# Performance work log

Measured on AMD Instinct MI355X. Metric: run time of the kernel, lower is better.

Reference implementation:

```python
import jax, jax.numpy as jnp
import numpy as np
from jax import lax

N_TAPS = 27  # 3x3x3 kernel

def _gather_one(xb, ti, hi, wi):
    # xb: (C,T,H,W); ti/hi/wi: (T,H,W) int32. Zero-fill outside bounds.
    C, T, H, W = xb.shape
    valid = (ti >= 0) & (ti < T) & (hi >= 0) & (hi < H) & (wi >= 0) & (wi < W)
    lin = (jnp.clip(ti, 0, T - 1) * H + jnp.clip(hi, 0, H - 1)) * W + jnp.clip(wi, 0, W - 1)
    v = jnp.take(xb.reshape(C, -1), lin.reshape(-1), axis=1).reshape(C, T, H, W)
    return v * valid.astype(xb.dtype)

_gather = jax.vmap(_gather_one)  # over batch

def _trilinear(x, t, h, w):
    # x: (B,C,T,H,W); t/h/w: (B,T,H,W) float sample coordinates.
    t0, h0, w0 = jnp.floor(t), jnp.floor(h), jnp.floor(w)
    lt, lh, lw = t - t0, h - h0, w - w0
    t0i, h0i, w0i = t0.astype(jnp.int32), h0.astype(jnp.int32), w0.astype(jnp.int32)
    acc = 0.0
    for ti, wt in ((t0i, 1.0 - lt), (t0i + 1, lt)):
        for hi, wh in ((h0i, 1.0 - lh), (h0i + 1, lh)):
            for wi, ww in ((w0i, 1.0 - lw), (w0i + 1, lw)):
                acc = acc + _gather(x, ti, hi, wi) * (wt * wh * ww)[:, None]
    return acc  # (B,C,T,H,W)

def _deform_conv3d(x, offset_w, offset_b, weight):
    # x: (B,Cin,T,H,W). Offset layout: (B, 3, 27, T, H, W), axis1=(dt,dh,dw),
    # tap index k = kt*9 + kh*3 + kw. stride=1, padding=1, dilation=1, no bias.
    off = lax.conv_general_dilated(
        x, offset_w, (1, 1, 1), [(1, 1)] * 3,
        dimension_numbers=("NCDHW", "OIDHW", "NCDHW"))
    off = off + offset_b[None, :, None, None, None]
    B, _, T, H, W = off.shape
    off = off.reshape(B, 3, N_TAPS, T, H, W)
    tg = jnp.arange(T, dtype=x.dtype)[:, None, None]
    hg = jnp.arange(H, dtype=x.dtype)[None, :, None]
    wg = jnp.arange(W, dtype=x.dtype)[None, None, :]
    out = jnp.zeros((B, weight.shape[0], T, H, W), x.dtype)
    for k in range(N_TAPS):
        kt, kh, kw = k // 9, (k // 3) % 3, k % 3
        t = tg + (kt - 1) + off[:, 0, k]
        h = hg + (kh - 1) + off[:, 1, k]
        w = wg + (kw - 1) + off[:, 2, k]
        s = _trilinear(x, t, h, w)  # (B,Cin,T,H,W)
        out = out + jnp.einsum('bcthw,oc->bothw', s, weight[:, :, kt, kh, kw])
    return out

def setup_inputs() -> dict:
    key = jax.random.key(0)
    ks = jax.random.split(key, 4)
    B, T, C, H, W = 1, 4, 64, 128, 128
    x = jax.random.normal(ks[0], (B, T, C, H, W), jnp.float32)
    # small init scale keeps predicted offsets in a realistic +-2px range
    offset_w = jax.random.normal(ks[1], (3 * N_TAPS, C, 3, 3, 3), jnp.float32) * 0.02
    offset_b = jnp.zeros((3 * N_TAPS,), jnp.float32)
    weight = jax.random.normal(ks[2], (C, C, 3, 3, 3), jnp.float32) * 0.02
    gamma = jax.random.normal(ks[3], (1,), jnp.float32) * 0.1
    return {"x": x, "offset_w": offset_w, "offset_b": offset_b,
            "weight": weight, "gamma": gamma}

def reference(x, offset_w, offset_b, weight, gamma):
    xp = jnp.transpose(x, (0, 2, 1, 3, 4))  # (B,C,T,H,W)
    xc = _deform_conv3d(xp, offset_w, offset_b, weight)
    return gamma[0] * jnp.transpose(xc, (0, 2, 1, 3, 4)) + x
```

## Files before the change

kernel.cpp:

```cpp
#include <hip/hip_runtime.h>
#include <cmath>

#define Cc 64
#define Hh 128
#define Ww 128
#define HW_ 16384
#define THW_ 65536
#define CHW_ 1048576
#define NT 27

typedef unsigned short ushort_t;
typedef _Float16 f16x2 __attribute__((ext_vector_type(2)));
typedef _Float16 f16x8 __attribute__((ext_vector_type(8)));
typedef __fp16 fp16x2_alt __attribute__((ext_vector_type(2)));
typedef float floatx4 __attribute__((ext_vector_type(4)));
typedef unsigned uint4v __attribute__((ext_vector_type(4)));

union U32H2 { unsigned u; f16x2 h; };

static __device__ inline ushort_t f2h(float f) {
  union { _Float16 h; ushort_t u; } v;
  v.h = (_Float16)f;
  return v.u;
}

static __device__ inline unsigned pk2(float a) {
  union { fp16x2_alt h; unsigned u; } v;
  v.h = __builtin_amdgcn_cvt_pkrtz(a, a);
  return v.u;
}

#if defined(__has_builtin)
#if __has_builtin(__builtin_amdgcn_make_buffer_rsrc) && __has_builtin(__builtin_amdgcn_raw_buffer_load_b32) && __has_builtin(__builtin_amdgcn_raw_buffer_load_b128)
#define USE_BUF 1
#endif
#endif
#ifndef USE_BUF
#define USE_BUF 0
#endif

struct XtBuf {
#if USE_BUF
  __amdgpu_buffer_rsrc_t r;
#else
  const char* p;
#endif
};

static __device__ inline XtBuf mkbuf(const ushort_t* xt) {
  XtBuf b;
#if USE_BUF
  b.r = __builtin_amdgcn_make_buffer_rsrc((void*)xt, (short)0, 8388608, 0x00020000);
#else
  b.p = (const char*)xt;
#endif
  return b;
}

static __device__ inline uint4v xload4(const XtBuf& b, unsigned voff) {
#if USE_BUF
  return __builtin_amdgcn_raw_buffer_load_b128(b.r, (int)voff, 0, 0);
#else
  return *(const uint4v*)(b.p + voff);
#endif
}


__global__ __launch_bounds__(256) void prep(
    const float* __restrict__ offset_w,
    const float* __restrict__ weight,
    ushort_t* __restrict__ w2frag,
    ushort_t* __restrict__ wfrag)
{
  int e = blockIdx.x * 256 + threadIdx.x;
  if (e < 165888) {
    int j = e & 7, ln = (e >> 3) & 63, kh2 = (e >> 9) & 1, r = e >> 10;
    int ot = r % 6, k = r / 6;
    int oc = ot * 16 + (ln & 15);
    int c  = kh2 * 32 + (ln >> 4) * 8 + j;
    float v = (oc < 81) ? offset_w[(oc * 64 + c) * 27 + k] : 0.f;
    w2frag[e] = f2h(v);
  }
  if (e < 110592) {
    int j = e & 7, ln = (e >> 3) & 63, kh2 = (e >> 9) & 1, r = e >> 10;
    int ot = r & 3, k = r >> 2;
    int o = ot * 16 + (ln & 15);
    int c = kh2 * 32 + (ln >> 4) * 8 + j;
    wfrag[e] = f2h(weight[(o * 64 + c) * 27 + k]);
  }
}

__global__ __launch_bounds__(256) void transpose_x(
    const float* __restrict__ x, ushort_t* __restrict__ xt)
{
  __shared__ float tile[64][65];
  int b = blockIdx.x;
  int wblk = b & 1;
  int th = b >> 1;
  int h = th & 127;
  int t = th >> 7;
  int w0 = wblk * 64;
  int lane = threadIdx.x & 63;
  int quad = threadIdx.x >> 6;
  #pragma unroll
  for (int cc = 0; cc < 16; ++cc) {
    int c = cc * 4 + quad;
    tile[c][lane] = x[t * CHW_ + c * HW_ + h * Ww + w0 + lane];
  }
  __syncthreads();
  #pragma unroll
  for (int ww = 0; ww < 16; ++ww) {
    int w = ww * 4 + quad;
    xt[(size_t)(t * HW_ + h * Ww + w0 + w) * 64 + lane] = f2h(tile[lane][w]);
  }
}

__global__ __launch_bounds__(256, 4) void offconv(
    const ushort_t* __restrict__ xt,
    const ushort_t* __restrict__ w2frag,
    const float* __restrict__ ob,
    float* __restrict__ off)
{
  __shared__ __align__(16) char lds[24960];
  ushort_t* S = (ushort_t*)lds;
  float* Dbuf = (float*)lds;
  int lane = threadIdx.x & 63;
  int wavei = __builtin_amdgcn_readfirstlane(threadIdx.x >> 6);
  int quad = lane >> 4;
  int m16 = lane & 15;
  int g8 = lane >> 3;
  unsigned coff = (unsigned)((lane & 7) * 16);
  int bid0 = blockIdx.x;
  int p0 = ((bid0 & 7) * 128 + (bid0 >> 3)) * 64;
  int t = p0 >> 14;
  int h = (p0 >> 7) & 127;
  int w0 = p0 & 127;
  XtBuf xb = mkbuf(xt);

  floatx4 acc[6];
  #pragma unroll
  for (int i = 0; i < 6; ++i) acc[i] = (floatx4){0.f, 0.f, 0.f, 0.f};

  uint4v pd[2];

  auto issue = [&](int k) {
    int kt = k / 9, kh = (k / 3) % 3, kw = k % 3;
    int ts = t + kt - 1, hs = h + kh - 1;
    int tsc = min(max(ts, 0), 3);
    int hsc = min(max(hs, 0), 127);
    int sbase = tsc * HW_ + hsc * Ww;
    #pragma unroll
    for (int b = 0; b < 2; ++b) {
      int prow = wavei * 16 + b * 8 + g8;
      int wc = w0 + prow + kw - 1;
      int wcc = min(max(wc, 0), 127);
      pd[b] = xload4(xb, ((unsigned)(sbase + wcc) << 7) + coff);
    }
  };

  issue(0);
  #pragma unroll 1
  for (int k = 0; k < NT; ++k) {
    int kt = k / 9, kh = (k / 3) % 3, kw = k % 3;
    int ts = t + kt - 1, hs = h + kh - 1;
    bool rowok = ((unsigned)ts < 4u) && ((unsigned)hs < 128u);
    #pragma unroll
    for (int b = 0; b < 2; ++b) {
      int prow = wavei * 16 + b * 8 + g8;
      int wc = w0 + prow + kw - 1;
      bool ok = rowok && ((unsigned)wc < 128u);
      uint4v v = pd[b];
      if (!ok) v = (uint4v){0u, 0u, 0u, 0u};
      *(uint4v*)((char*)S + prow * 144 + coff) = v;
    }
    issue(k + 1 < NT ? k + 1 : NT - 1);
    const ushort_t* srow = S + (wavei * 16 + m16) * 72 + quad * 8;
    f16x8 af0 = *(const f16x8*)srow;
    f16x8 af1 = *(const f16x8*)(srow + 32);
    #pragma unroll
    for (int ot = 0; ot < 6; ++ot) {
      const ushort_t* wb = w2frag + (size_t)((k * 6 + ot) * 2) * 512 + lane * 8;
      f16x8 b0 = *(const f16x8*)(wb);
      f16x8 b1 = *(const f16x8*)(wb + 512);
      acc[ot] = __builtin_amdgcn_mfma_f32_16x16x32_f16(af0, b0, acc[ot], 0, 0, 0);
      acc[ot] = __builtin_amdgcn_mfma_f32_16x16x32_f16(af1, b1, acc[ot], 0, 0, 0);
    }
  }
  __syncthreads();
  #pragma unroll
  for (int ot = 0; ot < 6; ++ot)
    #pragma unroll
    for (int r = 0; r < 4; ++r)
      Dbuf[(ot * 16 + m16) * 65 + wavei * 16 + quad * 4 + r] = acc[ot][r];
  __syncthreads();
  for (int i = threadIdx.x; i < 81 * 64; i += 256) {
    int oc = i >> 6, p = i & 63;
    off[(size_t)oc * THW_ + p0 + p] = Dbuf[oc * 65 + p] + ob[oc];
  }
}

#define SITE(W, D, A0, A1, A2, A3) \
  { U32H2 wu; wu.u = (W); U32H2 q0, q1, q2, q3; \
    q0.u = (D)[0]; q1.u = (D)[1]; q2.u = (D)[2]; q3.u = (D)[3]; \
    A0 += wu.h * q0.h; A1 += wu.h * q1.h; A2 += wu.h * q2.h; A3 += wu.h * q3.h; }

__global__ __launch_bounds__(256, 4) void deform(
    const float* __restrict__ x,
    const ushort_t* __restrict__ xt,
    const float* __restrict__ off,
    const ushort_t* __restrict__ wfrag,
    const float* __restrict__ gamma,
    float* __restrict__ out)
{
  __shared__ __align__(16) char lds[17408];
  ushort_t* S = (ushort_t*)lds;
  unsigned* msite0 = (unsigned*)(lds + 9216);
  unsigned* msite1 = (unsigned*)(lds + 11264);
  unsigned* mwt0   = (unsigned*)(lds + 13312);
  unsigned* mwt1   = (unsigned*)(lds + 15360);
  float* Dbuf = (float*)lds;
  int lane = threadIdx.x & 63;
  int wavei = __builtin_amdgcn_readfirstlane(threadIdx.x >> 6);
  int quad = lane >> 4;
  int m16 = lane & 15;
  int g8 = lane >> 3;
  unsigned coff = (unsigned)((lane & 7) * 16);
  int bid0 = blockIdx.x;
  int p0 = ((bid0 & 7) * 128 + (bid0 >> 3)) * 64;
  int t = p0 >> 14;
  int h = (p0 >> 7) & 127;
  int w0 = p0 & 127;
  XtBuf xb = mkbuf(xt);

  floatx4 acc[4];
  #pragma unroll
  for (int i = 0; i < 4; ++i) acc[i] = (floatx4){0.f, 0.f, 0.f, 0.f};

  int pl = wavei * 16 + m16;
  int pm = p0 + pl;
  int aq = quad >> 1, bq = quad & 1;
  int rowA = wavei * 16 + g8;
  int rowB = rowA + 8;
  const float* offT = off + pm;

  uint4v stA[8], stB[8];

  auto meta = [&](int kk, float dtv, float dhv, float dwv) {
    unsigned* ms = (kk & 1) ? msite1 : msite0;
    unsigned* mw = (kk & 1) ? mwt1 : mwt0;
    int kt = kk / 9, kh = (kk / 3) % 3, kw = kk % 3;
    float tf = (float)(t + kt - 1) + dtv;
    float hf = (float)(h + kh - 1) + dhv;
    float wf = (float)(w0 + pl + kw - 1) + dwv;
    float tF = floorf(tf), hF = floorf(hf), wF = floorf(wf);
    float lt = tf - tF, lh_ = hf - hF, lw_ = wf - wF;
    int t0 = (int)tF, h0 = (int)hF, wq_ = (int)wF;
    int ti = t0 + aq;
    float wt_ = (aq ? lt : 1.f - lt) * (((unsigned)ti < 4u) ? 1.f : 0.f);
    int tic = min(max(ti, 0), 3);
    int hi = h0 + bq;
    float wh_ = (bq ? lh_ : 1.f - lh_) * (((unsigned)hi < 128u) ? 1.f : 0.f);
    int hic = min(max(hi, 0), 127);
    int base2 = tic * HW_ + hic * Ww;
    float bw = wt_ * wh_;
    int wi0 = wq_;
    float ww0 = (1.f - lw_) * (((unsigned)wi0 < 128u) ? 1.f : 0.f);
    int wi0c = min(max(wi0, 0), 127);
    int wi1 = wq_ + 1;
    float ww1 = lw_ * (((unsigned)wi1 < 128u) ? 1.f : 0.f);
    int wi1c = min(max(wi1, 0), 127);
    uint2 sp_;
    sp_.x = (unsigned)(base2 + wi0c) << 7;
    sp_.y = (unsigned)(base2 + wi1c) << 7;
    *(uint2*)&ms[pl * 8 + quad * 2] = sp_;
    uint2 wp_;
    wp_.x = pk2(bw * ww0);
    wp_.y = pk2(bw * ww1);
    *(uint2*)&mw[pl * 8 + quad * 2] = wp_;
  };

  auto issueA = [&](int kk) {
    const unsigned* ms = (kk & 1) ? msite1 : msite0;
    const uint4* sp = (const uint4*)&ms[rowA * 8];
    uint4 s0 = sp[0], s1 = sp[1];
    stA[0] = xload4(xb, s0.x + coff);
    stA[1] = xload4(xb, s0.y + coff);
    stA[2] = xload4(xb, s0.z + coff);
    stA[3] = xload4(xb, s0.w + coff);
    stA[4] = xload4(xb, s1.x + coff);
    stA[5] = xload4(xb, s1.y + coff);
    stA[6] = xload4(xb, s1.z + coff);
    stA[7] = xload4(xb, s1.w + coff);
  };
  auto issueB = [&](int kk) {
    const unsigned* ms = (kk & 1) ? msite1 : msite0;
    const uint4* sp = (const uint4*)&ms[rowB * 8];
    uint4 s0 = sp[0], s1 = sp[1];
    stB[0] = xload4(xb, s0.x + coff);
    stB[1] = xload4(xb, s0.y + coff);
    stB[2] = xload4(xb, s0.z + coff);
    stB[3] = xload4(xb, s0.w + coff);
    stB[4] = xload4(xb, s1.x + coff);
    stB[5] = xload4(xb, s1.y + coff);
    stB[6] = xload4(xb, s1.z + coff);
    stB[7] = xload4(xb, s1.w + coff);
  };

  auto consumeA = [&](int kk) {
    const unsigned* mw = (kk & 1) ? mwt1 : mwt0;
    const uint4* wp = (const uint4*)&mw[rowA * 8];
    uint4 w03 = wp[0], w47 = wp[1];
    U32H2 z; z.u = 0;
    f16x2 e0 = z.h, e1 = z.h, e2 = z.h, e3 = z.h;
    f16x2 o0 = z.h, o1 = z.h, o2 = z.h, o3 = z.h;
    SITE(w03.x, stA[0], e0, e1, e2, e3)
    SITE(w03.y, stA[1], o0, o1, o2, o3)
    SITE(w03.z, stA[2], e0, e1, e2, e3)
    SITE(w03.w, stA[3], o0, o1, o2, o3)
    SITE(w47.x, stA[4], e0, e1, e2, e3)
    SITE(w47.y, stA[5], o0, o1, o2, o3)
    SITE(w47.z, stA[6], e0, e1, e2, e3)
    SITE(w47.w, stA[7], o0, o1, o2, o3)
    U32H2 r0, r1, r2, r3;
    r0.h = e0 + o0; r1.h = e1 + o1; r2.h = e2 + o2; r3.h = e3 + o3;
    uint4v res = {r0.u, r1.u, r2.u, r3.u};
    *(uint4v*)((char*)S + rowA * 144 + coff) = res;
  };
  auto consumeB = [&](int kk) {
    const unsigned* mw = (kk & 1) ? mwt1 : mwt0;
    const uint4* wp = (const uint4*)&mw[rowB * 8];
    uint4 w03 = wp[0], w47 = wp[1];
    U32H2 z; z.u = 0;
    f16x2 e0 = z.h, e1 = z.h, e2 = z.h, e3 = z.h;
    f16x2 o0 = z.h, o1 = z.h, o2 = z.h, o3 = z.h;
    SITE(w03.x, stB[0], e0, e1, e2, e3)
    SITE(w03.y, stB[1], o0, o1, o2, o3)
    SITE(w03.z, stB[2], e0, e1, e2, e3)
    SITE(w03.w, stB[3], o0, o1, o2, o3)
    SITE(w47.x, stB[4], e0, e1, e2, e3)
    SITE(w47.y, stB[5], o0, o1, o2, o3)
    SITE(w47.z, stB[6], e0, e1, e2, e3)
    SITE(w47.w, stB[7], o0, o1, o2, o3)
    U32H2 r0, r1, r2, r3;
    r0.h = e0 + o0; r1.h = e1 + o1; r2.h = e2 + o2; r3.h = e3 + o3;
    uint4v res = {r0.u, r1.u, r2.u, r3.u};
    *(uint4v*)((char*)S + rowB * 144 + coff) = res;
  };

  float dt0 = offT[(size_t)(0 * NT + 0) * THW_];
  float dh0 = offT[(size_t)(1 * NT + 0) * THW_];
  float dw0 = offT[(size_t)(2 * NT + 0) * THW_];
  meta(0, dt0, dh0, dw0);
  issueA(0);

  #pragma unroll 1
  for (int k = 0; k < NT; ++k) {
    int kn = (k + 1 < NT) ? k + 1 : NT - 1;
    float dt_n = offT[(size_t)(0 * NT + kn) * THW_];
    float dh_n = offT[(size_t)(1 * NT + kn) * THW_];
    float dw_n = offT[(size_t)(2 * NT + kn) * THW_];

    issueB(k);
    __builtin_amdgcn_sched_barrier(0);
    consumeA(k);
    meta(kn, dt_n, dh_n, dw_n);
    consumeB(k);
    issueA(kn);
    __builtin_amdgcn_sched_barrier(0);

    const ushort_t* srow = S + (wavei * 16 + m16) * 72 + quad * 8;
    f16x8 af0 = *(const f16x8*)srow;
    f16x8 af1 = *(const f16x8*)(srow + 32);
    #pragma unroll
    for (int ot = 0; ot < 4; ++ot) {
      const ushort_t* wb = wfrag + (size_t)((k * 4 + ot) * 2) * 512 + lane * 8;
      f16x8 b0 = *(const f16x8*)(wb);
      f16x8 b1 = *(const f16x8*)(wb + 512);
      acc[ot] = __builtin_amdgcn_mfma_f32_16x16x32_f16(af0, b0, acc[ot], 0, 0, 0);
      acc[ot] = __builtin_amdgcn_mfma_f32_16x16x32_f16(af1, b1, acc[ot], 0, 0, 0);
    }
  }
  __syncthreads();
  #pragma unroll
  for (int ot = 0; ot < 4; ++ot)
    #pragma unroll
    for (int r = 0; r < 4; ++r)
      Dbuf[(ot * 16 + m16) * 65 + wavei * 16 + quad * 4 + r] = acc[ot][r];
  __syncthreads();
  float g = gamma[0];
  for (int i = threadIdx.x; i < 64 * 64; i += 256) {
    int oc = i >> 6, p = i & 63;
    size_t oi = (size_t)t * CHW_ + (size_t)oc * HW_ + (size_t)h * Ww + w0 + p;
    out[oi] = fmaf(g, Dbuf[oc * 65 + p], x[oi]);
  }
}

extern "C" void kernel_launch(void* const* d_in, const int* in_sizes, int n_in,
                              void* d_out, int out_size, void* d_ws, size_t ws_size,
                              hipStream_t stream) {
  (void)in_sizes; (void)n_in; (void)out_size; (void)ws_size;
  const float* x        = (const float*)d_in[0];
  const float* offset_w = (const float*)d_in[1];
  const float* offset_b = (const float*)d_in[2];
  const float* weight   = (const float*)d_in[3];
  const float* gamma    = (const float*)d_in[4];
  float* out = (float*)d_out;
  float* wsf = (float*)d_ws;
  float*    off    = wsf;
  ushort_t* xt     = (ushort_t*)(wsf + 5308416);
  ushort_t* wfrag  = (ushort_t*)(wsf + 7405568);
  ushort_t* w2frag = (ushort_t*)(wsf + 7460864);

  hipLaunchKernelGGL(prep, dim3(648), dim3(256), 0, stream,
                     offset_w, weight, w2frag, wfrag);
  hipLaunchKernelGGL(transpose_x, dim3(1024), dim3(256), 0, stream, x, xt);
  hipLaunchKernelGGL(offconv, dim3(1024), dim3(256), 0, stream,
                     xt, w2frag, offset_b, off);
  hipLaunchKernelGGL(deform, dim3(1024), dim3(256), 0, stream,
                     x, xt, off, wfrag, gamma, out);
}
```

Before: 224.6 us.

## Fuse offset convolution into deformable conv kernel, keeping offsets in LDS

Merges the offset-prediction conv kernel and the deformable sampling kernel into one launch. Each block computes its 81 offset channels for its 64 pixels with MFMA, adds the bias, and keeps them in shared memory instead of writing them to and reading them back from a global workspace. This removes a global round trip of about 21 MB and one kernel launch. In exchange LDS per block grows to about 38 KB, which may lower occupancy, and register pressure rises because both phases live in one kernel.

```diff
diff --git a/kernel.cpp b/kernel.cpp
--- a/kernel.cpp
+++ b/kernel.cpp
@@ -115,14 +115,27 @@
   }
 }
 
-__global__ __launch_bounds__(256, 4) void offconv(
+#define SITE(W, D, A0, A1, A2, A3) \
+  { U32H2 wu; wu.u = (W); U32H2 q0, q1, q2, q3; \
+    q0.u = (D)[0]; q1.u = (D)[1]; q2.u = (D)[2]; q3.u = (D)[3]; \
+    A0 += wu.h * q0.h; A1 += wu.h * q1.h; A2 += wu.h * q2.h; A3 += wu.h * q3.h; }
+
+__global__ __launch_bounds__(256, 4) void fused(
+    const float* __restrict__ x,
     const ushort_t* __restrict__ xt,
     const ushort_t* __restrict__ w2frag,
     const float* __restrict__ ob,
-    float* __restrict__ off)
+    const ushort_t* __restrict__ wfrag,
+    const float* __restrict__ gamma,
+    float* __restrict__ out)
 {
-  __shared__ __align__(16) char lds[24960];
+  __shared__ __align__(16) char lds[38480];
   ushort_t* S = (ushort_t*)lds;
+  unsigned* msite0 = (unsigned*)(lds + 9216);
+  unsigned* msite1 = (unsigned*)(lds + 11264);
+  unsigned* mwt0   = (unsigned*)(lds + 13312);
+  unsigned* mwt1   = (unsigned*)(lds + 15360);
+  float* Obuf = (float*)(lds + 17408);
   float* Dbuf = (float*)lds;
   int lane = threadIdx.x & 63;
   int wavei = __builtin_amdgcn_readfirstlane(threadIdx.x >> 6);
@@ -137,111 +150,76 @@
   int w0 = p0 & 127;
   XtBuf xb = mkbuf(xt);
 
-  floatx4 acc[6];
-  #pragma unroll
-  for (int i = 0; i < 6; ++i) acc[i] = (floatx4){0.f, 0.f, 0.f, 0.f};
-
-  uint4v pd[2];
-
-  auto issue = [&](int k) {
-    int kt = k / 9, kh = (k / 3) % 3, kw = k % 3;
-    int ts = t + kt - 1, hs = h + kh - 1;
-    int tsc = min(max(ts, 0), 3);
-    int hsc = min(max(hs, 0), 127);
-    int sbase = tsc * HW_ + hsc * Ww;
+  {
+    floatx4 acc[6];
     #pragma unroll
-    for (int b = 0; b < 2; ++b) {
-      int prow = wavei * 16 + b * 8 + g8;
-      int wc = w0 + prow + kw - 1;
-      int wcc = min(max(wc, 0), 127);
-      pd[b] = xload4(xb, ((unsigned)(sbase + wcc) << 7) + coff);
+    for (int i = 0; i < 6; ++i) acc[i] = (floatx4){0.f, 0.f, 0.f, 0.f};
+
+    uint4v pd[2];
+
+    auto issue = [&](int k) {
+      int kt = k / 9, kh = (k / 3) % 3, kw = k % 3;
+      int ts = t + kt - 1, hs = h + kh - 1;
+      int tsc = min(max(ts, 0), 3);
+      int hsc = min(max(hs, 0), 127);
+      int sbase = tsc * HW_ + hsc * Ww;
+      #pragma unroll
+      for (int b = 0; b < 2; ++b) {
+        int prow = wavei * 16 + b * 8 + g8;
+        int wc = w0 + prow + kw - 1;
+        int wcc = min(max(wc, 0), 127);
+        pd[b] = xload4(xb, ((unsigned)(sbase + wcc) << 7) + coff);
+      }
+    };
+
+    issue(0);
+    #pragma unroll 1
+    for (int k = 0; k < NT; ++k) {
+      int kt = k / 9, kh = (k / 3) % 3, kw = k % 3;
+      int ts = t + kt - 1, hs = h + kh - 1;
+      bool rowok = ((unsigned)ts < 4u) && ((unsigned)hs < 128u);
+      #pragma unroll
+      for (int b = 0; b < 2; ++b) {
+        int prow = wavei * 16 + b * 8 + g8;
+        int wc = w0 + prow + kw - 1;
+        bool ok = rowok && ((unsigned)wc < 128u);
+        uint4v v = pd[b];
+        if (!ok) v = (uint4v){0u, 0u, 0u, 0u};
+        *(uint4v*)((char*)S + prow * 144 + coff) = v;
+      }
+      if (k + 1 < NT) issue(k + 1);
+      const ushort_t* srow = S + (wavei * 16 + m16) * 72 + quad * 8;
+      f16x8 af0 = *(const f16x8*)srow;
+      f16x8 af1 = *(const f16x8*)(srow + 32);
+      #pragma unroll
+      for (int ot = 0; ot < 6; ++ot) {
+        const ushort_t* wb = w2frag + (size_t)((k * 6 + ot) * 2) * 512 + lane * 8;
+        f16x8 b0 = *(const f16x8*)(wb);
+        f16x8 b1 = *(const f16x8*)(wb + 512);
+        acc[ot] = __builtin_amdgcn_mfma_f32_16x16x32_f16(af0, b0, acc[ot], 0, 0, 0);
+        acc[ot] = __builtin_amdgcn_mfma_f32_16x16x32_f16(af1, b1, acc[ot], 0, 0, 0);
+      }
     }
-  };
-
-  issue(0);
-  #pragma unroll 1
-  for (int k = 0; k < NT; ++k) {
-    int kt = k / 9, kh = (k / 3) % 3, kw = k % 3;
-    int ts = t + kt - 1, hs = h + kh - 1;
-    bool rowok = ((unsigned)ts < 4u) && ((unsigned)hs < 128u);
-    #pragma unroll
-    for (int b = 0; b < 2; ++b) {
-      int prow = wavei * 16 + b * 8 + g8;
-      int wc = w0 + prow + kw - 1;
-      bool ok = rowok && ((unsigned)wc < 128u);
-      uint4v v = pd[b];
-      if (!ok) v = (uint4v){0u, 0u, 0u, 0u};
-      *(uint4v*)((char*)S + prow * 144 + coff) = v;
-    }
-    issue(k + 1 < NT ? k + 1 : NT - 1);
-    const ushort_t* srow = S + (wavei * 16 + m16) * 72 + quad * 8;
-    f16x8 af0 = *(const f16x8*)srow;
-    f16x8 af1 = *(const f16x8*)(srow + 32);
     #pragma unroll
     for (int ot = 0; ot < 6; ++ot) {
-      const ushort_t* wb = w2frag + (size_t)((k * 6 + ot) * 2) * 512 + lane * 8;
-      f16x8 b0 = *(const f16x8*)(wb);
-      f16x8 b1 = *(const f16x8*)(wb + 512);
-      acc[ot] = __builtin_amdgcn_mfma_f32_16x16x32_f16(af0, b0, acc[ot], 0, 0, 0);
-      acc[ot] = __builtin_amdgcn_mfma_f32_16x16x32_f16(af1, b1, acc[ot], 0, 0, 0);
+      int oc = ot * 16 + m16;
+      if (oc < 81) {
+        float bv = ob[oc];
+        #pragma unroll
+        for (int r = 0; r < 4; ++r)
+          Obuf[oc * 65 + wavei * 16 + quad * 4 + r] = acc[ot][r] + bv;
+      }
     }
   }
-  __syncthreads();
-  #pragma unroll
-  for (int ot = 0; ot < 6; ++ot)
-    #pragma unroll
-    for (int r = 0; r < 4; ++r)
-      Dbuf[(ot * 16 + m16) * 65 + wavei * 16 + quad * 4 + r] = acc[ot][r];
-  __syncthreads();
-  for (int i = threadIdx.x; i < 81 * 64; i += 256) {
-    int oc = i >> 6, p = i & 63;
-    off[(size_t)oc * THW_ + p0 + p] = Dbuf[oc * 65 + p] + ob[oc];
-  }
-}
-
-#define SITE(W, D, A0, A1, A2, A3) \
-  { U32H2 wu; wu.u = (W); U32H2 q0, q1, q2, q3; \
-    q0.u = (D)[0]; q1.u = (D)[1]; q2.u = (D)[2]; q3.u = (D)[3]; \
-    A0 += wu.h * q0.h; A1 += wu.h * q1.h; A2 += wu.h * q2.h; A3 += wu.h * q3.h; }
-
-__global__ __launch_bounds__(256, 4) void deform(
-    const float* __restrict__ x,
-    const ushort_t* __restrict__ xt,
-    const float* __restrict__ off,
-    const ushort_t* __restrict__ wfrag,
-    const float* __restrict__ gamma,
-    float* __restrict__ out)
-{
-  __shared__ __align__(16) char lds[17408];
-  ushort_t* S = (ushort_t*)lds;
-  unsigned* msite0 = (unsigned*)(lds + 9216);
-  unsigned* msite1 = (unsigned*)(lds + 11264);
-  unsigned* mwt0   = (unsigned*)(lds + 13312);
-  unsigned* mwt1   = (unsigned*)(lds + 15360);
-  float* Dbuf = (float*)lds;
-  int lane = threadIdx.x & 63;
-  int wavei = __builtin_amdgcn_readfirstlane(threadIdx.x >> 6);
-  int quad = lane >> 4;
-  int m16 = lane & 15;
-  int g8 = lane >> 3;
-  unsigned coff = (unsigned)((lane & 7) * 16);
-  int bid0 = blockIdx.x;
-  int p0 = ((bid0 & 7) * 128 + (bid0 >> 3)) * 64;
-  int t = p0 >> 14;
-  int h = (p0 >> 7) & 127;
-  int w0 = p0 & 127;
-  XtBuf xb = mkbuf(xt);
 
   floatx4 acc[4];
   #pragma unroll
   for (int i = 0; i < 4; ++i) acc[i] = (floatx4){0.f, 0.f, 0.f, 0.f};
 
   int pl = wavei * 16 + m16;
-  int pm = p0 + pl;
   int aq = quad >> 1, bq = quad & 1;
   int rowA = wavei * 16 + g8;
   int rowB = rowA + 8;
-  const float* offT = off + pm;
 
   uint4v stA[8], stB[8];
 
@@ -347,25 +325,27 @@
     *(uint4v*)((char*)S + rowB * 144 + coff) = res;
   };
 
-  float dt0 = offT[(size_t)(0 * NT + 0) * THW_];
-  float dh0 = offT[(size_t)(1 * NT + 0) * THW_];
-  float dw0 = offT[(size_t)(2 * NT + 0) * THW_];
-  meta(0, dt0, dh0, dw0);
+  {
+    float dt0 = Obuf[(0 * NT + 0) * 65 + pl];
+    float dh0 = Obuf[(1 * NT + 0) * 65 + pl];
+    float dw0 = Obuf[(2 * NT + 0) * 65 + pl];
+    meta(0, dt0, dh0, dw0);
+  }
   issueA(0);
 
   #pragma unroll 1
   for (int k = 0; k < NT; ++k) {
     int kn = (k + 1 < NT) ? k + 1 : NT - 1;
-    float dt_n = offT[(size_t)(0 * NT + kn) * THW_];
-    float dh_n = offT[(size_t)(1 * NT + kn) * THW_];
-    float dw_n = offT[(size_t)(2 * NT + kn) * THW_];
+    float dt_n = Obuf[(0 * NT + kn) * 65 + pl];
+    float dh_n = Obuf[(1 * NT + kn) * 65 + pl];
+    float dw_n = Obuf[(2 * NT + kn) * 65 + pl];
 
     issueB(k);
     __builtin_amdgcn_sched_barrier(0);
     consumeA(k);
-    meta(kn, dt_n, dh_n, dw_n);
+    if (k + 1 < NT) meta(kn, dt_n, dh_n, dw_n);
     consumeB(k);
-    issueA(kn);
+    if (k + 1 < NT) issueA(kn);
     __builtin_amdgcn_sched_barrier(0);
 
     const ushort_t* srow = S + (wavei * 16 + m16) * 72 + quad * 8;
@@ -406,7 +386,6 @@
   const float* gamma    = (const float*)d_in[4];
   float* out = (float*)d_out;
   float* wsf = (float*)d_ws;
-  float*    off    = wsf;
   ushort_t* xt     = (ushort_t*)(wsf + 5308416);
   ushort_t* wfrag  = (ushort_t*)(wsf + 7405568);
   ushort_t* w2frag = (ushort_t*)(wsf + 7460864);
@@ -414,8 +393,6 @@
   hipLaunchKernelGGL(prep, dim3(648), dim3(256), 0, stream,
                      offset_w, weight, w2frag, wfrag);
   hipLaunchKernelGGL(transpose_x, dim3(1024), dim3(256), 0, stream, x, xt);
-  hipLaunchKernelGGL(offconv, dim3(1024), dim3(256), 0, stream,
-                     xt, w2frag, offset_b, off);
-  hipLaunchKernelGGL(deform, dim3(1024), dim3(256), 0, stream,
-                     x, xt, off, wfrag, gamma, out);
-}
+  hipLaunchKernelGGL(fused, dim3(1024), dim3(256), 0, stream,
+                     x, xt, w2frag, offset_b, wfrag, gamma, out);
+}
```

Result: faster. 208.1 us (-7.3%).
